# Optimization experiments

Measured on AMD Instinct MI355X. Metric: run time of the kernel, lower is better.

## Reference

```python
import jax, jax.numpy as jnp
import numpy as np

B, V, C, H, W = 2, 8, 32, 256, 320


def setup_inputs() -> dict:
    key = jax.random.key(0)
    k1, k2, k3 = jax.random.split(key, 3)
    features = jax.random.normal(k1, (B, V, C, H, W), dtype=jnp.float32)
    # near-identity homographies so sampled coords are mostly in-bounds
    eye = jnp.eye(4, dtype=jnp.float32)
    projections = eye[None, None] + 0.05 * jax.random.normal(k2, (B, V, 4, 4), dtype=jnp.float32)
    depth_values = 0.5 + jax.random.uniform(k3, (B, H * W), dtype=jnp.float32)
    return {"features": features, "projections": projections, "depth_values": depth_values}


def grid_sample_bilinear_zeros(feat, grid):
    # feat: (N, C, H, W); grid: (N, H, W, 2) normalized coords in [-1, 1]
    # torch.nn.functional.grid_sample, mode='bilinear', padding_mode='zeros',
    # align_corners=False (torch default)
    N, Cc, Hh, Ww = feat.shape
    ix = (grid[..., 0] + 1.0) * (Ww * 0.5) - 0.5   # unnormalize, align_corners=False
    iy = (grid[..., 1] + 1.0) * (Hh * 0.5) - 0.5
    ix0 = jnp.floor(ix)
    iy0 = jnp.floor(iy)
    wx1 = ix - ix0
    wy1 = iy - iy0
    wx0 = 1.0 - wx1
    wy0 = 1.0 - wy1
    bidx = jnp.arange(N)[:, None, None]

    def gather(iyc, ixc):
        valid = (ixc >= 0) & (ixc <= Ww - 1) & (iyc >= 0) & (iyc <= Hh - 1)
        xs = jnp.clip(ixc, 0, Ww - 1).astype(jnp.int32)
        ys = jnp.clip(iyc, 0, Hh - 1).astype(jnp.int32)
        v = feat[bidx, :, ys, xs]          # (N, H, W, C)
        return v * valid[..., None].astype(feat.dtype)

    out = (gather(iy0, ix0) * (wx0 * wy0)[..., None]
           + gather(iy0, ix0 + 1) * (wx1 * wy0)[..., None]
           + gather(iy0 + 1, ix0) * (wx0 * wy1)[..., None]
           + gather(iy0 + 1, ix0 + 1) * (wx1 * wy1)[..., None])
    return jnp.transpose(out, (0, 3, 1, 2))   # (N, C, H, W)


def reference(features, projections, depth_values):
    b, v, c, h, w = features.shape
    rot = projections[:, :, :3, :3]            # (B, V, 3, 3)
    trans = projections[:, :, :3, 3:4]         # (B, V, 3, 1)
    if depth_values.ndim == 1:
        d = depth_values.reshape(b, 1, 1, 1)
    else:
        d = depth_values.reshape(b, 1, 1, h * w)
    x, y = jnp.meshgrid(jnp.arange(w, dtype=jnp.float32),
                        jnp.arange(h, dtype=jnp.float32), indexing='xy')
    cg = jnp.stack([x.ravel(), y.ravel(), jnp.ones(h * w, dtype=jnp.float32)])  # (3, HW)
    cg = jnp.einsum('bvij,jk->bvik', rot, cg) * d + trans                        # (B, V, 3, HW)
    xy = cg[:, :, :2, :] / cg[:, :, 2:3, :]
    gx = xy[:, :, 0, :] / (w - 1) * 2.0 - 1.0
    gy = xy[:, :, 1, :] / (h - 1) * 2.0 - 1.0
    grid = jnp.stack([gx, gy], axis=3).reshape(b * v, h, w, 2)
    grid = jax.lax.stop_gradient(grid)         # torch version computes grid under no_grad
    feat = features.reshape(b * v, c, h, w)
    out = grid_sample_bilinear_zeros(feat, grid)
    return out.reshape(b, v, c, h, w)
```

## Files before the change

### kernel.cpp

```cpp
#include <hip/hip_runtime.h>

#define B_ 2
#define V_ 8
#define C_ 32
#define H_ 256
#define W_ 320
#define HW_ (H_ * W_)

__global__ __launch_bounds__(256) void feature_projector_kernel(
    const float* __restrict__ features,
    const float* __restrict__ projections,
    const float* __restrict__ depth,
    float* __restrict__ out)
{
    const int n = blockIdx.y;
    const int b = n >> 3;
    const int pix = blockIdx.x * blockDim.x + threadIdx.x;

    const int xi = pix % W_;
    const int yi = pix / W_;
    const float xf = (float)xi;
    const float yf = (float)yi;

    const float* P = projections + n * 16;
    const float r00 = P[0], r01 = P[1], r02 = P[2],  t0 = P[3];
    const float r10 = P[4], r11 = P[5], r12 = P[6],  t1 = P[7];
    const float r20 = P[8], r21 = P[9], r22 = P[10], t2 = P[11];

    const float d = depth[b * HW_ + pix];

    const float cx = (r00 * xf + r01 * yf + r02) * d + t0;
    const float cy = (r10 * xf + r11 * yf + r12) * d + t1;
    const float cz = (r20 * xf + r21 * yf + r22) * d + t2;

    const float px = cx / cz;
    const float py = cy / cz;
    const float gx = px / (float)(W_ - 1) * 2.0f - 1.0f;
    const float gy = py / (float)(H_ - 1) * 2.0f - 1.0f;

    const float ix = (gx + 1.0f) * ((float)W_ * 0.5f) - 0.5f;
    const float iy = (gy + 1.0f) * ((float)H_ * 0.5f) - 0.5f;

    const float ix0 = floorf(ix);
    const float iy0 = floorf(iy);
    const float ix1 = ix0 + 1.0f;
    const float iy1 = iy0 + 1.0f;

    const float wx1 = ix - ix0;
    const float wy1 = iy - iy0;
    const float wx0 = 1.0f - wx1;
    const float wy0 = 1.0f - wy1;

    const float fW1 = (float)(W_ - 1);
    const float fH1 = (float)(H_ - 1);

    const float vx0 = (ix0 >= 0.0f && ix0 <= fW1) ? 1.0f : 0.0f;
    const float vx1 = (ix1 >= 0.0f && ix1 <= fW1) ? 1.0f : 0.0f;
    const float vy0 = (iy0 >= 0.0f && iy0 <= fH1) ? 1.0f : 0.0f;
    const float vy1 = (iy1 >= 0.0f && iy1 <= fH1) ? 1.0f : 0.0f;

    const int xb  = (int)fminf(fmaxf(ix0, 0.0f), (float)(W_ - 2));
    const int x0c = (int)fminf(fmaxf(ix0, 0.0f), fW1);
    const int x1c = (int)fminf(fmaxf(ix1, 0.0f), fW1);
    const int y0c = (int)fminf(fmaxf(iy0, 0.0f), fH1);
    const int y1c = (int)fminf(fmaxf(iy1, 0.0f), fH1);

    const float wxa = wx0 * vx0;
    const float wxb = wx1 * vx1;
    const float a0 = (x0c == xb     ? wxa : 0.0f) + (x1c == xb     ? wxb : 0.0f);
    const float a1 = (x0c == xb + 1 ? wxa : 0.0f) + (x1c == xb + 1 ? wxb : 0.0f);
    const float ry0 = wy0 * vy0;
    const float ry1 = wy1 * vy1;

    const int r0 = y0c * W_ + xb;
    const int r1 = y1c * W_ + xb;

    const float* __restrict__ fN = features + (size_t)n * C_ * HW_;
    float* __restrict__ oN = out + (size_t)n * C_ * HW_ + pix;

#pragma unroll 8
    for (int c = 0; c < C_; ++c) {
        const float* __restrict__ fc = fN + (size_t)c * HW_;
        float2 p0, p1;
        __builtin_memcpy(&p0, fc + r0, 8);
        __builtin_memcpy(&p1, fc + r1, 8);
        const float v = (p0.x * a0 + p0.y * a1) * ry0
                      + (p1.x * a0 + p1.y * a1) * ry1;
        oN[(size_t)c * HW_] = v;
    }
}

extern "C" void kernel_launch(void* const* d_in, const int* in_sizes, int n_in,
                              void* d_out, int out_size, void* d_ws, size_t ws_size,
                              hipStream_t stream) {
    const float* features    = (const float*)d_in[0];
    const float* projections = (const float*)d_in[1];
    const float* depth       = (const float*)d_in[2];
    float* out = (float*)d_out;

    dim3 block(256, 1, 1);
    dim3 grid(HW_ / 256, B_ * V_, 1);
    feature_projector_kernel<<<grid, block, 0, stream>>>(features, projections, depth, out);
}
```

Measured before the change: 350.2 us.

## Double-buffer channel gathers in software pipeline with sched barriers

Replaces the unrolled channel loop with a two-stage software pipeline. Two banks of 8-channel float2 gathers are kept in registers, so 16 channels of loads are in flight while the previous bank is computed and stored. sched_barrier calls pin this ordering against the compiler scheduler. Launch bounds now request 4 blocks per CU to cap register use. The cost is higher register pressure, which may reduce occupancy or cause spills.

```diff
diff --git a/kernel.cpp b/kernel.cpp
--- a/kernel.cpp
+++ b/kernel.cpp
@@ -7,7 +7,7 @@
 #define W_ 320
 #define HW_ (H_ * W_)
 
-__global__ __launch_bounds__(256) void feature_projector_kernel(
+__global__ __launch_bounds__(256, 4) void feature_projector_kernel(
     const float* __restrict__ features,
     const float* __restrict__ projections,
     const float* __restrict__ depth,
@@ -78,16 +78,42 @@
     const float* __restrict__ fN = features + (size_t)n * C_ * HW_;
     float* __restrict__ oN = out + (size_t)n * C_ * HW_ + pix;
 
-#pragma unroll 8
-    for (int c = 0; c < C_; ++c) {
-        const float* __restrict__ fc = fN + (size_t)c * HW_;
-        float2 p0, p1;
-        __builtin_memcpy(&p0, fc + r0, 8);
-        __builtin_memcpy(&p1, fc + r1, 8);
-        const float v = (p0.x * a0 + p0.y * a1) * ry0
-                      + (p1.x * a0 + p1.y * a1) * ry1;
-        oN[(size_t)c * HW_] = v;
+    float2 pa0[8], pa1[8], pb0[8], pb1[8];
+
+#define LOADB(dst0, dst1, c0)                                            \
+    {                                                                    \
+        _Pragma("unroll")                                                \
+        for (int j = 0; j < 8; ++j) {                                    \
+            const float* __restrict__ fc = fN + (size_t)((c0) + j) * HW_;\
+            __builtin_memcpy(&dst0[j], fc + r0, 8);                      \
+            __builtin_memcpy(&dst1[j], fc + r1, 8);                      \
+        }                                                                \
     }
+
+#define COMPB(src0, src1, c0)                                            \
+    {                                                                    \
+        _Pragma("unroll")                                                \
+        for (int j = 0; j < 8; ++j) {                                    \
+            const float v = (src0[j].x * a0 + src0[j].y * a1) * ry0      \
+                          + (src1[j].x * a0 + src1[j].y * a1) * ry1;     \
+            oN[(size_t)((c0) + j) * HW_] = v;                            \
+        }                                                                \
+    }
+
+    LOADB(pa0, pa1, 0)
+    LOADB(pb0, pb1, 8)
+    __builtin_amdgcn_sched_barrier(0);
+    COMPB(pa0, pa1, 0)
+    LOADB(pa0, pa1, 16)
+    __builtin_amdgcn_sched_barrier(0);
+    COMPB(pb0, pb1, 8)
+    LOADB(pb0, pb1, 24)
+    __builtin_amdgcn_sched_barrier(0);
+    COMPB(pa0, pa1, 16)
+    COMPB(pb0, pb1, 24)
+
+#undef LOADB
+#undef COMPB
 }
 
 extern "C" void kernel_launch(void* const* d_in, const int* in_sizes, int n_in,
```

Result: faster. 327.7 us (-6.4%).

## Software-pipeline channel loop with barrier-synced waves, larger blocks, XCD-aware block remap

Applied to the files above, without the earlier changes.

Raises the block size to 1024 threads and remaps block indices so that consecutive blocks, which on MI355X are dispatched round-robin across XCDs, work on nearby pixel ranges. The channel loop becomes a two-deep software pipeline with scheduling barriers, plus a workgroup barrier each iteration that keeps the waves of a block in step so their gathers share cache lines. Output stores are now nontemporal so the write stream does not evict feature data from cache. The risks are that the per-iteration s_barrier stalls all waves on the slowest one, and that unroll 1 with explicit double buffering may expose less memory-level parallelism than the earlier unroll of 8.

```diff
diff --git a/kernel.cpp b/kernel.cpp
--- a/kernel.cpp
+++ b/kernel.cpp
@@ -6,8 +6,10 @@
 #define H_ 256
 #define W_ 320
 #define HW_ (H_ * W_)
+#define TPB_ 1024
+#define BLK_X_ (HW_ / TPB_)
 
-__global__ __launch_bounds__(256) void feature_projector_kernel(
+__global__ __launch_bounds__(TPB_, 8) void feature_projector_kernel(
     const float* __restrict__ features,
     const float* __restrict__ projections,
     const float* __restrict__ depth,
@@ -15,7 +17,9 @@
 {
     const int n = blockIdx.y;
     const int b = n >> 3;
-    const int pix = blockIdx.x * blockDim.x + threadIdx.x;
+
+    const int bidx = (blockIdx.x & 7) * (BLK_X_ / 8) + (blockIdx.x >> 3);
+    const int pix = bidx * TPB_ + threadIdx.x;
 
     const int xi = pix % W_;
     const int yi = pix / W_;
@@ -78,16 +82,40 @@
     const float* __restrict__ fN = features + (size_t)n * C_ * HW_;
     float* __restrict__ oN = out + (size_t)n * C_ * HW_ + pix;
 
-#pragma unroll 8
-    for (int c = 0; c < C_; ++c) {
-        const float* __restrict__ fc = fN + (size_t)c * HW_;
-        float2 p0, p1;
-        __builtin_memcpy(&p0, fc + r0, 8);
-        __builtin_memcpy(&p1, fc + r1, 8);
-        const float v = (p0.x * a0 + p0.y * a1) * ry0
-                      + (p1.x * a0 + p1.y * a1) * ry1;
-        oN[(size_t)c * HW_] = v;
+    float2 qa0, qa1, qb0, qb1;
+
+#define LOADC(d0, d1, c)                                                 \
+    {                                                                    \
+        const float* __restrict__ fc = fN + (size_t)(c) * HW_;           \
+        __builtin_memcpy(&d0, fc + r0, 8);                               \
+        __builtin_memcpy(&d1, fc + r1, 8);                               \
     }
+#define COMPC(s0, s1, c)                                                 \
+    {                                                                    \
+        const float v = (s0.x * a0 + s0.y * a1) * ry0                    \
+                      + (s1.x * a0 + s1.y * a1) * ry1;                   \
+        __builtin_nontemporal_store(v, &oN[(size_t)(c) * HW_]);          \
+    }
+
+    LOADC(qa0, qa1, 0)
+    LOADC(qb0, qb1, 1)
+    __builtin_amdgcn_sched_barrier(0);
+
+#pragma unroll 1
+    for (int c = 0; c < C_ - 2; c += 2) {
+        __builtin_amdgcn_s_barrier();
+        COMPC(qa0, qa1, c)
+        LOADC(qa0, qa1, c + 2)
+        __builtin_amdgcn_sched_barrier(0);
+        COMPC(qb0, qb1, c + 1)
+        LOADC(qb0, qb1, c + 3)
+        __builtin_amdgcn_sched_barrier(0);
+    }
+    COMPC(qa0, qa1, C_ - 2)
+    COMPC(qb0, qb1, C_ - 1)
+
+#undef LOADC
+#undef COMPC
 }
 
 extern "C" void kernel_launch(void* const* d_in, const int* in_sizes, int n_in,
@@ -98,7 +126,7 @@
     const float* depth       = (const float*)d_in[2];
     float* out = (float*)d_out;
 
-    dim3 block(256, 1, 1);
-    dim3 grid(HW_ / 256, B_ * V_, 1);
+    dim3 block(TPB_, 1, 1);
+    dim3 grid(BLK_X_, B_ * V_, 1);
     feature_projector_kernel<<<grid, block, 0, stream>>>(features, projections, depth, out);
 }
```

Result: no change. 350.2 us (+0.0%).
